# Kernel optimization log

Measured on AMD Instinct MI355X. Metric: run time of the kernel, lower is better.

## Reference

```python
import jax, jax.numpy as jnp
import numpy as np

N = 512      # num_nodes
T = 12       # seq_len
D = 1        # input_shape1
H = 64       # rnn_units
ED = 10      # units (node embedding dim)
K = 2        # cheb_k
B = 64       # batch
OUT = 1      # output_dim


def setup_inputs() -> dict:
    key = jax.random.key(0)
    ks = jax.random.split(key, 14)
    s = 0.1
    gts = jax.random.normal(ks[0], (B, N, T, D), jnp.float32)
    u = jax.random.uniform(ks[1], (N, N, 2), jnp.float32, 1e-6, 1.0 - 1e-6)
    gumbel_noise = -jnp.log(-jnp.log(u))
    node_embeddings = jax.random.normal(ks[2], (N, ED), jnp.float32)
    gate_w0 = jax.random.normal(ks[3], (ED, K, D + H, 2 * H), jnp.float32) * s
    gate_b0 = jax.random.normal(ks[4], (ED, 2 * H), jnp.float32) * s
    upd_w0 = jax.random.normal(ks[5], (ED, K, D + H, H), jnp.float32) * s
    upd_b0 = jax.random.normal(ks[6], (ED, H), jnp.float32) * s
    gate_w1 = jax.random.normal(ks[7], (ED, K, H + H, 2 * H), jnp.float32) * s
    gate_b1 = jax.random.normal(ks[8], (ED, 2 * H), jnp.float32) * s
    upd_w1 = jax.random.normal(ks[9], (ED, K, H + H, H), jnp.float32) * s
    upd_b1 = jax.random.normal(ks[10], (ED, H), jnp.float32) * s
    conv_w = jax.random.normal(ks[11], (T * OUT, H), jnp.float32) * s  # Conv2d(1, T*OUT, (1,H)) kernel flattened
    conv_b = jax.random.normal(ks[12], (T * OUT,), jnp.float32) * s
    return dict(gts=gts, gumbel_noise=gumbel_noise, node_embeddings=node_embeddings,
                gate_w0=gate_w0, gate_b0=gate_b0, upd_w0=upd_w0, upd_b0=upd_b0,
                gate_w1=gate_w1, gate_b1=gate_b1, upd_w1=upd_w1, upd_b1=upd_b1,
                conv_w=conv_w, conv_b=conv_b)


def _gconv(x, supports, E, Wp, bp):
    # x: [B,N,i], supports: [K,N,N], node-adaptive weights from pools
    xg = jnp.einsum('knm,bmi->bnki', supports, x)          # cheb graph conv
    W = jnp.einsum('nd,dkio->nkio', E, Wp)                 # per-node weights
    b = E @ bp                                             # [N,o]
    return jnp.einsum('bnki,nkio->bno', xg, W) + b


def _cell(x, h, supports, E, gw, gb, uw, ub):
    zr = jax.nn.sigmoid(_gconv(jnp.concatenate([x, h], -1), supports, E, gw, gb))
    z, r = jnp.split(zr, 2, axis=-1)
    hc = jnp.tanh(_gconv(jnp.concatenate([x, z * h], -1), supports, E, uw, ub))
    return r * h + (1.0 - r) * hc


def _scaled_laplacian(E, gumbel_noise):
    lg = E @ E.T
    nrm = jnp.linalg.norm(E, axis=1, keepdims=True)
    lg = lg / (nrm @ nrm.T)
    lg = (lg + 1.0) / 2.0
    logits = jnp.stack([lg, 1.0 - lg], axis=-1)
    y_soft = jax.nn.softmax(logits + gumbel_noise, axis=-1)  # tau=1
    y_hard = jax.nn.one_hot(jnp.argmax(y_soft, axis=-1), 2, dtype=y_soft.dtype)
    y = y_hard + y_soft - jax.lax.stop_gradient(y_soft)      # straight-through
    eye = jnp.eye(N, dtype=y.dtype)
    adj = y[..., 0] * (1.0 - eye)                            # zero diagonal
    d = adj.sum(axis=1)
    L = jnp.diag(d) - adj
    lmax = L.max() - L.min()
    tilde = 2.0 * L / lmax - eye
    return adj, tilde


def reference(gts, gumbel_noise, node_embeddings, gate_w0, gate_b0, upd_w0, upd_b0,
              gate_w1, gate_b1, upd_w1, upd_b1, conv_w, conv_b):
    E = node_embeddings
    _, tilde = _scaled_laplacian(E, gumbel_noise)
    eye = jnp.eye(N, dtype=tilde.dtype)
    supports = jnp.stack([eye, tilde])                       # cheb_k = 2
    x = jnp.transpose(gts, (0, 2, 1, 3))                     # [B,T,N,D]
    cur = jnp.moveaxis(x, 1, 0)                              # [T,B,N,D]
    b = gts.shape[0]
    for gw, gb, uw, ub in ((gate_w0, gate_b0, upd_w0, upd_b0),
                           (gate_w1, gate_b1, upd_w1, upd_b1)):
        h0 = jnp.zeros((b, N, uw.shape[-1]), dtype=gts.dtype)
        def step(h, xt, gw=gw, gb=gb, uw=uw, ub=ub):
            hn = _cell(xt, h, supports, E, gw, gb, uw, ub)
            return hn, hn
        _, cur = jax.lax.scan(step, h0, cur)                 # [T,B,N,H]
    last = cur[-1]                                           # [B,N,H] (output[:, -1])
    y = jnp.einsum('bnh,oh->bon', last, conv_w) + conv_b[None, :, None]  # end_conv
    out = y.reshape(b, T, OUT, N).transpose(0, 1, 3, 2)      # [B,T,N,OUT]
    return out
```

## Files before the change

kernel.cpp:

```cpp
#include <hip/hip_runtime.h>
#include <math.h>

#define NN 512
#define TSEQ 12
#define BB 64

typedef unsigned short u16;
typedef short s16x4 __attribute__((ext_vector_type(4)));
typedef short s16x8 __attribute__((ext_vector_type(8)));
typedef float f32x4 __attribute__((ext_vector_type(4)));

__device__ __forceinline__ float b2f(u16 h) { return __uint_as_float(((unsigned)h) << 16); }
__device__ __forceinline__ u16 f2b(float f) {
    unsigned u = __float_as_uint(f);
    return (u16)((u + 0x7FFFu + ((u >> 16) & 1u)) >> 16);
}

constexpr size_t SZP    = (size_t)512 * 4096 * 2;
constexpr size_t B_ADJ  = 0;
constexpr size_t B_DD   = B_ADJ + 524288;
constexpr size_t B_NRM  = B_DD + 2048;
constexpr size_t B_LMAX = B_NRM + 2048;
constexpr size_t B_XSH  = B_LMAX + 256;
constexpr size_t B_XSL  = B_XSH + 786432;
constexpr size_t B_TXH  = B_XSL + 786432;
constexpr size_t B_TXL  = B_TXH + 786432;
constexpr size_t B_ST   = B_TXL + 786432;
constexpr size_t B_RBUF = B_ST + 12 * SZP;
constexpr size_t B_G0TH = B_RBUF + 8388608;
constexpr size_t B_G0TL = B_G0TH + 16777216;
constexpr size_t B_U0TH = B_G0TL + 16777216;
constexpr size_t B_U0TL = B_U0TH + 8388608;
constexpr size_t B_G1TH = B_U0TL + 8388608;
constexpr size_t B_G1TL = B_G1TH + 33554432;
constexpr size_t B_U1TH = B_G1TL + 33554432;
constexpr size_t B_U1TL = B_U1TH + 16777216;
constexpr size_t B_BG0  = B_U1TL + 16777216;
constexpr size_t B_BU0  = B_BG0 + 262144;
constexpr size_t B_BG1  = B_BU0 + 131072;
constexpr size_t B_BU1  = B_BG1 + 262144;
constexpr size_t B_G0X  = B_BU1 + 131072;
constexpr size_t B_U0X  = B_G0X + 524288;
constexpr size_t WS_BYTES = B_U0X + 262144;


__global__ void k_marker(float* out, float v) { out[threadIdx.x] = v; }

__global__ void k_norm(const float* __restrict__ E, float* __restrict__ nrm) {
    int n = blockIdx.x * blockDim.x + threadIdx.x;
    if (n < NN) {
        float s = 0.f;
        #pragma unroll
        for (int q = 0; q < 10; ++q) { float e = E[n * 10 + q]; s += e * e; }
        nrm[n] = sqrtf(s);
    }
}

__global__ __launch_bounds__(256) void k_adj(const float* __restrict__ E, const float* __restrict__ gn,
                                             const float* __restrict__ nrm, u16* __restrict__ adjb,
                                             float* __restrict__ dd) {
    __shared__ float En[10];
    __shared__ float red[256];
    int n = blockIdx.x, tid = threadIdx.x;
    if (tid < 10) En[tid] = E[n * 10 + tid];
    __syncthreads();
    float nn = nrm[n];
    float cnt = 0.f;
    for (int m = tid; m < NN; m += 256) {
        float dot = 0.f;
        #pragma unroll
        for (int q = 0; q < 10; ++q) dot += En[q] * E[m * 10 + q];
        float lg = dot / (nn * nrm[m]);
        lg = (lg + 1.f) * 0.5f;
        float g0 = gn[((size_t)n * NN + m) * 2 + 0];
        float g1 = gn[((size_t)n * NN + m) * 2 + 1];
        bool a = ((lg + g0) >= (1.f - lg + g1) && (m != n));
        adjb[(size_t)n * NN + m] = a ? 0x3F80 : 0;
        cnt += a ? 1.f : 0.f;
    }
    red[tid] = cnt;
    __syncthreads();
    for (int s = 128; s > 0; s >>= 1) { if (tid < s) red[tid] += red[tid + s]; __syncthreads(); }
    if (tid == 0) dd[n] = red[0];
}

__global__ void k_dmax(const float* __restrict__ dd, float* __restrict__ lmax) {
    __shared__ float red[512];
    int t = threadIdx.x;
    red[t] = dd[t];
    __syncthreads();
    for (int s = 256; s > 0; s >>= 1) { if (t < s) red[t] = fmaxf(red[t], red[t + s]); __syncthreads(); }
    if (t == 0) lmax[0] = red[0] + (red[0] > 0.f ? 1.f : 0.f);
}

__global__ __launch_bounds__(256) void k_xs_bf(const float* __restrict__ gts, u16* __restrict__ xh,
                                               u16* __restrict__ xl) {
    int idx = blockIdx.x * 256 + threadIdx.x;
    if (idx >= NN * TSEQ * BB) return;
    int n = idx / (TSEQ * BB);
    int rem = idx - n * (TSEQ * BB);
    int t = rem >> 6, b = rem & 63;
    float v = gts[((size_t)b * NN + n) * TSEQ + t];
    u16 hb = f2b(v);
    xh[idx] = hb;
    xl[idx] = f2b(v - b2f(hb));
}

template <int K2, int O, bool SHIFT>
__global__ __launch_bounds__(256) void k_embed2(const float* __restrict__ E, const float* __restrict__ Wp,
                                                u16* __restrict__ oh, u16* __restrict__ ol) {
    constexpr int KR = SHIFT ? 130 : K2;
    constexpr int NKB = K2 / 32;
    __shared__ float WpL[10][32][33];
    __shared__ float eL[16][10];
    const int nc = blockIdx.x, kc = blockIdx.y, oc = blockIdx.z;
    const int tid = threadIdx.x;
    const int rb = kc * 32 + (SHIFT ? (kc >= 2 ? 2 : 1) : 0);
    const int ocol = oc * 32;
    const int n0 = nc * 16;

    for (int el = tid; el < 10 * 32 * 32; el += 256) {
        int d = el >> 10;
        int rem = el & 1023;
        int k = rem >> 5, o = rem & 31;
        WpL[d][k][o] = Wp[((size_t)d * KR + rb + k) * O + ocol + o];
    }
    if (tid < 160) eL[tid / 10][tid % 10] = E[(n0 + tid / 10) * 10 + tid % 10];
    __syncthreads();

    const int o2 = tid >> 3;
    const int kv = (tid & 7) * 4;
    const int o = ocol + o2;
    const int lane = ((kv >> 3) << 4) + (o & 15);
    const size_t fragbase =
        ((((size_t)0 * (O / 16) + (o >> 4)) * NKB + kc) * 64 + lane) * 8 + (kv & 7);
    const size_t nstride = (size_t)(O / 16) * NKB * 64 * 8;

    for (int ni = 0; ni < 16; ++ni) {
        float ev[10];
        #pragma unroll
        for (int d = 0; d < 10; ++d) ev[d] = eL[ni][d];
        u16 ph[4], pl[4];
        #pragma unroll
        for (int j = 0; j < 4; ++j) {
            float a = 0.f;
            #pragma unroll
            for (int d = 0; d < 10; ++d) a += ev[d] * WpL[d][kv + j][o2];
            u16 hb = f2b(a);
            ph[j] = hb;
            pl[j] = f2b(a - b2f(hb));
        }
        size_t off = fragbase + (size_t)(n0 + ni) * nstride;
        *(s16x4*)&oh[off] = *(s16x4*)ph;
        *(s16x4*)&ol[off] = *(s16x4*)pl;
    }
}

__global__ __launch_bounds__(256) void k_bias(const float* __restrict__ E, const float* __restrict__ gb0,
                                              const float* __restrict__ ub0, const float* __restrict__ gb1,
                                              const float* __restrict__ ub1, const float* __restrict__ gw0,
                                              const float* __restrict__ uw0,
                                              float* BG0, float* BU0, float* BG1, float* BU1,
                                              float* G0X, float* U0X) {
    __shared__ float e[10];
    int n = blockIdx.x, tid = threadIdx.x;
    if (tid < 10) e[tid] = E[n * 10 + tid];
    __syncthreads();
    if (tid < 128) {
        int o = tid;
        float a0 = 0, a1 = 0, a2 = 0, a3 = 0;
        #pragma unroll
        for (int d = 0; d < 10; ++d) {
            a0 += e[d] * gb0[d * 128 + o];
            a1 += e[d] * gb1[d * 128 + o];
            a2 += e[d] * gw0[((size_t)d * 130 + 0) * 128 + o];
            a3 += e[d] * gw0[((size_t)d * 130 + 65) * 128 + o];
        }
        BG0[n * 128 + o] = a0; BG1[n * 128 + o] = a1;
        G0X[n * 256 + o] = a2; G0X[n * 256 + 128 + o] = a3;
    } else if (tid < 192) {
        int o = tid - 128;
        float a0 = 0, a1 = 0, a2 = 0, a3 = 0;
        #pragma unroll
        for (int d = 0; d < 10; ++d) {
            a0 += e[d] * ub0[d * 64 + o];
            a1 += e[d] * ub1[d * 64 + o];
            a2 += e[d] * uw0[((size_t)d * 130 + 0) * 64 + o];
            a3 += e[d] * uw0[((size_t)d * 130 + 65) * 64 + o];
        }
        BU0[n * 64 + o] = a0; BU1[n * 64 + o] = a1;
        U0X[n * 128 + o] = a2; U0X[n * 128 + 64 + o] = a3;
    }
}

__global__ __launch_bounds__(256) void k_gmm(const u16* __restrict__ A, const u16* __restrict__ Bh,
                                             const u16* __restrict__ Bl, const float* __restrict__ dd,
                                             const float* __restrict__ lmax,
                                             u16* __restrict__ Ch, u16* __restrict__ Cl, int N) {
    __shared__ u16 As[2][64][72];
    __shared__ u16 Bsh[2][2][64][32];
    __shared__ u16 Bsl[2][2][64][32];
    const int tid = threadIdx.x;
    const int w = tid >> 6, l = tid & 63, lr = l & 15, lg = l >> 4;
    const int bm = blockIdx.y * 64, bn = blockIdx.x * 64;
    const int am = tid >> 2, ak = (tid & 3) * 16;
    const int bk = tid >> 3, bn8 = (tid & 7) * 8;
    const int bx = (tid & 7) & 3;
    const int col = ((bk >> 3) ^ bx) * 8 + (bk & 7);
    f32x4 acc[4];
    #pragma unroll
    for (int a = 0; a < 4; ++a) acc[a] = (f32x4){0.f, 0.f, 0.f, 0.f};

    const int nl = w * 16 + lr;
    const int cc = (lg ^ ((nl >> 3) & 3)) * 8;
    const size_t arow = (size_t)(bm + am) * 512;

    s16x8 rA0, rA1, rBh[2], rBl[2];
    rA0 = *(const s16x8*)&A[arow + 0 + ak];
    rA1 = *(const s16x8*)&A[arow + 0 + ak + 8];
    #pragma unroll
    for (int hh = 0; hh < 2; ++hh) {
        rBh[hh] = *(const s16x8*)&Bh[(size_t)(0 + hh * 32 + bk) * N + bn + bn8];
        rBl[hh] = *(const s16x8*)&Bl[(size_t)(0 + hh * 32 + bk) * N + bn + bn8];
    }
    *(s16x8*)&As[0][am][ak]     = rA0;
    *(s16x8*)&As[0][am][ak + 8] = rA1;
    #pragma unroll
    for (int hh = 0; hh < 2; ++hh) {
        #pragma unroll
        for (int q = 0; q < 8; ++q) {
            Bsh[0][hh][bn8 + q][col] = ((const u16*)&rBh[hh])[q];
            Bsl[0][hh][bn8 + q][col] = ((const u16*)&rBl[hh])[q];
        }
    }
    __syncthreads();

    for (int k0 = 0; k0 < 512; k0 += 64) {
        const int cur = (k0 >> 6) & 1;
        const bool more = (k0 + 64 < 512);
        if (more) {
            rA0 = *(const s16x8*)&A[arow + k0 + 64 + ak];
            rA1 = *(const s16x8*)&A[arow + k0 + 64 + ak + 8];
            #pragma unroll
            for (int hh = 0; hh < 2; ++hh) {
                rBh[hh] = *(const s16x8*)&Bh[(size_t)(k0 + 64 + hh * 32 + bk) * N + bn + bn8];
                rBl[hh] = *(const s16x8*)&Bl[(size_t)(k0 + 64 + hh * 32 + bk) * N + bn + bn8];
            }
        }
        #pragma unroll
        for (int hh = 0; hh < 2; ++hh) {
            s16x8 bfh = *(const s16x8*)&Bsh[cur][hh][nl][cc];
            s16x8 bfl = *(const s16x8*)&Bsl[cur][hh][nl][cc];
            #pragma unroll
            for (int mf = 0; mf < 4; ++mf) {
                s16x8 afr = *(const s16x8*)&As[cur][mf * 16 + lr][hh * 32 + lg * 8];
                acc[mf] = __builtin_amdgcn_mfma_f32_16x16x32_bf16(afr, bfh, acc[mf], 0, 0, 0);
                acc[mf] = __builtin_amdgcn_mfma_f32_16x16x32_bf16(afr, bfl, acc[mf], 0, 0, 0);
            }
        }
        if (more) {
            const int nxt = cur ^ 1;
            *(s16x8*)&As[nxt][am][ak]     = rA0;
            *(s16x8*)&As[nxt][am][ak + 8] = rA1;
            #pragma unroll
            for (int hh = 0; hh < 2; ++hh) {
                #pragma unroll
                for (int q = 0; q < 8; ++q) {
                    Bsh[nxt][hh][bn8 + q][col] = ((const u16*)&rBh[hh])[q];
                    Bsl[nxt][hh][bn8 + q][col] = ((const u16*)&rBl[hh])[q];
                }
            }
        }
        __syncthreads();
    }
    const float lm = lmax[0], alpha = -2.f / lm;
    const int colg = bn + w * 16 + lr;
    #pragma unroll
    for (int mf = 0; mf < 4; ++mf) {
        #pragma unroll
        for (int i = 0; i < 4; ++i) {
            int rowg = bm + mf * 16 + lg * 4 + i;
            size_t off = (size_t)rowg * N + colg;
            float hval = b2f(Bh[off]) + b2f(Bl[off]);
            float beta = 2.f * dd[rowg] / lm - 1.f;
            float v = alpha * acc[mf][i] + beta * hval;
            u16 hb = f2b(v);
            Ch[off] = hb;
            Cl[off] = f2b(v - b2f(hb));
        }
    }
}

struct CellP {
    const u16 *s0h, *s0l, *s1h, *s1l, *s2h, *s2l, *s3h, *s3l;
    const u16 *Wh, *Wl;
    const float *bias, *wx;
    const u16 *xsh, *xsl, *txh, *txl;
    const u16 *hph, *hpl;
    float* rbuf;
    u16 *oh, *ol;
    int xoff;
};
template <int K2, int O, bool GATE, bool RANK1>
__global__ __launch_bounds__(256) void k_cellp(CellP p) {
    constexpr int NKB = K2 / 32;
    constexpr int MFW = (O == 128) ? 4 : 2;
    const int n = blockIdx.x, tid = threadIdx.x;
    const int w = tid >> 6, l = tid & 63, lr = l & 15, lg = l >> 4;
    const int mbase = (O == 128) ? 0 : ((w >> 1) * 2);
    const int nbase = (O == 128) ? (2 * w) : ((w & 1) * 2);
    f32x4 acc[MFW][2];
    #pragma unroll
    for (int a = 0; a < MFW; ++a)
        #pragma unroll
        for (int c = 0; c < 2; ++c) acc[a][c] = (f32x4){0.f, 0.f, 0.f, 0.f};
    const size_t nb = (size_t)n * 4096;

    #pragma unroll
    for (int kb = 0; kb < NKB; ++kb) {
        const int sg = kb >> 1;
        const u16* sh = sg == 0 ? p.s0h : sg == 1 ? p.s1h : sg == 2 ? p.s2h : p.s3h;
        const u16* sl = sg == 0 ? p.s0l : sg == 1 ? p.s1l : sg == 2 ? p.s2l : p.s3l;
        const int koff = (kb & 1) * 32 + lg * 8;
        s16x8 bfh[2], bfl[2];
        #pragma unroll
        for (int nf = 0; nf < 2; ++nf) {
            size_t wof = ((((size_t)n * (O / 16) + (nbase + nf)) * NKB + kb) * 64 + l) * 8;
            bfh[nf] = *(const s16x8*)&p.Wh[wof];
            bfl[nf] = *(const s16x8*)&p.Wl[wof];
        }
        #pragma unroll
        for (int mf = 0; mf < MFW; ++mf) {
            int b = (mbase + mf) * 16 + lr;
            s16x8 ah = *(const s16x8*)&sh[nb + b * 64 + koff];
            s16x8 al = *(const s16x8*)&sl[nb + b * 64 + koff];
            #pragma unroll
            for (int nf = 0; nf < 2; ++nf) {
                acc[mf][nf] = __builtin_amdgcn_mfma_f32_16x16x32_bf16(ah, bfh[nf], acc[mf][nf], 0, 0, 0);
                acc[mf][nf] = __builtin_amdgcn_mfma_f32_16x16x32_bf16(ah, bfl[nf], acc[mf][nf], 0, 0, 0);
                acc[mf][nf] = __builtin_amdgcn_mfma_f32_16x16x32_bf16(al, bfh[nf], acc[mf][nf], 0, 0, 0);
            }
        }
    }

    const float* wxn = RANK1 ? (p.wx + (size_t)n * 2 * O) : p.wx;
    #pragma unroll
    for (int mf = 0; mf < MFW; ++mf) {
        #pragma unroll
        for (int i = 0; i < 4; ++i) {
            int b = (mbase + mf) * 16 + lg * 4 + i;
            float xf = 0.f, txf = 0.f;
            if (RANK1) {
                int idx = n * 768 + p.xoff + b;
                xf = b2f(p.xsh[idx]) + b2f(p.xsl[idx]);
                txf = b2f(p.txh[idx]) + b2f(p.txl[idx]);
            }
            #pragma unroll
            for (int nf = 0; nf < 2; ++nf) {
                int o = (nbase + nf) * 16 + lr;
                float s = acc[mf][nf][i] + p.bias[(size_t)n * O + o];
                if (RANK1) s += xf * wxn[o] + txf * wxn[O + o];
                size_t bo = nb + (size_t)b * 64;
                if (GATE) {
                    float v = 1.f / (1.f + expf(-s));
                    if (o < 64) {
                        float hp = b2f(p.hph[bo + o]) + b2f(p.hpl[bo + o]);
                        float zh = v * hp;
                        u16 hb = f2b(zh);
                        p.oh[bo + o] = hb;
                        p.ol[bo + o] = f2b(zh - b2f(hb));
                    } else {
                        p.rbuf[bo + (o - 64)] = v;
                    }
                } else {
                    float hc = tanhf(s);
                    float rv = p.rbuf[bo + o];
                    float hp = b2f(p.oh[bo + o]) + b2f(p.ol[bo + o]);
                    float hn = rv * hp + (1.f - rv) * hc;
                    u16 hb = f2b(hn);
                    p.oh[bo + o] = hb;
                    p.ol[bo + o] = f2b(hn - b2f(hb));
                }
            }
        }
    }
}

__global__ __launch_bounds__(256) void k_conv(const u16* __restrict__ hh, const u16* __restrict__ hl,
                                              const float* __restrict__ cw, const float* __restrict__ cb,
                                              float* __restrict__ out) {
    int idx = blockIdx.x * 256 + threadIdx.x;
    int n = idx >> 6, b = idx & 63;
    float hv[64];
    #pragma unroll
    for (int q = 0; q < 8; ++q) {
        s16x8 vh = *(const s16x8*)&hh[(size_t)n * 4096 + b * 64 + q * 8];
        s16x8 vl = *(const s16x8*)&hl[(size_t)n * 4096 + b * 64 + q * 8];
        #pragma unroll
        for (int j = 0; j < 8; ++j) hv[q * 8 + j] = b2f((u16)vh[j]) + b2f((u16)vl[j]);
    }
    #pragma unroll
    for (int t = 0; t < TSEQ; ++t) {
        float s = cb[t];
        #pragma unroll
        for (int j = 0; j < 64; ++j) s += hv[j] * cw[t * 64 + j];
        out[((size_t)b * TSEQ + t) * NN + n] = s;
    }
}

extern "C" void kernel_launch(void* const* d_in, const int* in_sizes, int n_in,
                              void* d_out, int out_size, void* d_ws, size_t ws_size,
                              hipStream_t stream) {
    const float* gts = (const float*)d_in[0];
    const float* gn  = (const float*)d_in[1];
    const float* E   = (const float*)d_in[2];
    const float* gw0 = (const float*)d_in[3];
    const float* gb0 = (const float*)d_in[4];
    const float* uw0 = (const float*)d_in[5];
    const float* ub0 = (const float*)d_in[6];
    const float* gw1 = (const float*)d_in[7];
    const float* gb1 = (const float*)d_in[8];
    const float* uw1 = (const float*)d_in[9];
    const float* ub1 = (const float*)d_in[10];
    const float* cw  = (const float*)d_in[11];
    const float* cb  = (const float*)d_in[12];
    float* out = (float*)d_out;
    char* ws = (char*)d_ws;

    if (ws_size < WS_BYTES) {
        k_marker<<<1, 64, 0, stream>>>(out, (float)(ws_size >> 20));
        return;
    }

    u16* adjb = (u16*)(ws + B_ADJ);
    float* dd = (float*)(ws + B_DD);
    float* nrm = (float*)(ws + B_NRM);
    float* lmax = (float*)(ws + B_LMAX);
    u16* xsh = (u16*)(ws + B_XSH);
    u16* xsl = (u16*)(ws + B_XSL);
    u16* txh = (u16*)(ws + B_TXH);
    u16* txl = (u16*)(ws + B_TXL);
    u16* h0h  = (u16*)(ws + B_ST + 0 * SZP);
    u16* h0l  = (u16*)(ws + B_ST + 1 * SZP);
    u16* h1h  = (u16*)(ws + B_ST + 2 * SZP);
    u16* h1l  = (u16*)(ws + B_ST + 3 * SZP);
    u16* th0h = (u16*)(ws + B_ST + 4 * SZP);
    u16* th0l = (u16*)(ws + B_ST + 5 * SZP);
    u16* th1h = (u16*)(ws + B_ST + 6 * SZP);
    u16* th1l = (u16*)(ws + B_ST + 7 * SZP);
    u16* zhh  = (u16*)(ws + B_ST + 8 * SZP);
    u16* zhl  = (u16*)(ws + B_ST + 9 * SZP);
    u16* tzh  = (u16*)(ws + B_ST + 10 * SZP);
    u16* tzl  = (u16*)(ws + B_ST + 11 * SZP);
    float* rbuf = (float*)(ws + B_RBUF);
    u16* G0TH = (u16*)(ws + B_G0TH);
    u16* G0TL = (u16*)(ws + B_G0TL);
    u16* U0TH = (u16*)(ws + B_U0TH);
    u16* U0TL = (u16*)(ws + B_U0TL);
    u16* G1TH = (u16*)(ws + B_G1TH);
    u16* G1TL = (u16*)(ws + B_G1TL);
    u16* U1TH = (u16*)(ws + B_U1TH);
    u16* U1TL = (u16*)(ws + B_U1TL);
    float* BG0 = (float*)(ws + B_BG0);
    float* BU0 = (float*)(ws + B_BU0);
    float* BG1 = (float*)(ws + B_BG1);
    float* BU1 = (float*)(ws + B_BU1);
    float* G0X = (float*)(ws + B_G0X);
    float* U0X = (float*)(ws + B_U0X);

    hipMemsetAsync(ws, 0, WS_BYTES, stream);

    k_norm<<<2, 256, 0, stream>>>(E, nrm);
    k_adj<<<NN, 256, 0, stream>>>(E, gn, nrm, adjb, dd);
    k_dmax<<<1, 512, 0, stream>>>(dd, lmax);

    k_xs_bf<<<(NN * TSEQ * BB + 255) / 256, 256, 0, stream>>>(gts, xsh, xsl);
    k_gmm<<<dim3(TSEQ * BB / 64, 8), 256, 0, stream>>>(adjb, xsh, xsl, dd, lmax, txh, txl, TSEQ * BB);

    k_embed2<128, 128, true><<<dim3(32, 4, 4), 256, 0, stream>>>(E, gw0, G0TH, G0TL);
    k_embed2<128, 64, true><<<dim3(32, 4, 2), 256, 0, stream>>>(E, uw0, U0TH, U0TL);
    k_embed2<256, 128, false><<<dim3(32, 8, 4), 256, 0, stream>>>(E, gw1, G1TH, G1TL);
    k_embed2<256, 64, false><<<dim3(32, 8, 2), 256, 0, stream>>>(E, uw1, U1TH, U1TL);
    k_bias<<<512, 256, 0, stream>>>(E, gb0, ub0, gb1, ub1, gw0, uw0,
                                    BG0, BU0, BG1, BU1, G0X, U0X);

    const dim3 gmm_grid(BB * 64 / 64, 8);
    for (int t = 0; t < TSEQ; ++t) {
        int xoff = t * BB;
        CellP g0{h0h, h0l, th0h, th0l, nullptr, nullptr, nullptr, nullptr,
                 G0TH, G0TL, BG0, G0X, xsh, xsl, txh, txl, h0h, h0l, rbuf, zhh, zhl, xoff};
        k_cellp<128, 128, true, true><<<NN, 256, 0, stream>>>(g0);
        k_gmm<<<gmm_grid, 256, 0, stream>>>(adjb, zhh, zhl, dd, lmax, tzh, tzl, 4096);
        CellP u0{zhh, zhl, tzh, tzl, nullptr, nullptr, nullptr, nullptr,
                 U0TH, U0TL, BU0, U0X, xsh, xsl, txh, txl, nullptr, nullptr, rbuf, h0h, h0l, xoff};
        k_cellp<128, 64, false, true><<<NN, 256, 0, stream>>>(u0);
        k_gmm<<<gmm_grid, 256, 0, stream>>>(adjb, h0h, h0l, dd, lmax, th0h, th0l, 4096);
        CellP g1{h0h, h0l, h1h, h1l, th0h, th0l, th1h, th1l,
                 G1TH, G1TL, BG1, nullptr, nullptr, nullptr, nullptr, nullptr, h1h, h1l, rbuf, zhh, zhl, 0};
        k_cellp<256, 128, true, false><<<NN, 256, 0, stream>>>(g1);
        k_gmm<<<gmm_grid, 256, 0, stream>>>(adjb, zhh, zhl, dd, lmax, tzh, tzl, 4096);
        CellP u1{h0h, h0l, zhh, zhl, th0h, th0l, tzh, tzl,
                 U1TH, U1TL, BU1, nullptr, nullptr, nullptr, nullptr, nullptr, nullptr, nullptr, rbuf, h1h, h1l, 0};
        k_cellp<256, 64, false, false><<<NN, 256, 0, stream>>>(u1);
        if (t + 1 < TSEQ)
            k_gmm<<<gmm_grid, 256, 0, stream>>>(adjb, h1h, h1l, dd, lmax, th1h, th1l, 4096);
    }

    k_conv<<<NN * BB / 256, 256, 0, stream>>>(h1h, h1l, cw, cb, out);
}
```

Measured before the change: 1.942 ms.

## Fuse layer-1 hidden graph conv with next step's layer-0 gate cell

Wraps the GEMM and cell kernels as device functions and adds a combined kernel. Its first 512 blocks compute the support product of the layer-1 hidden state, and the remaining 512 blocks compute the next timestep's layer-0 gate cell. The two are independent, so this removes one launch per step and lets them overlap on the GPU. The cell blocks now reserve the GEMM's shared memory even though they don't use it, which may reduce occupancy.

```diff
diff --git a/kernel.cpp b/kernel.cpp
--- a/kernel.cpp
+++ b/kernel.cpp
@@ -193,16 +193,19 @@
     }
 }
 
-__global__ __launch_bounds__(256) void k_gmm(const u16* __restrict__ A, const u16* __restrict__ Bh,
-                                             const u16* __restrict__ Bl, const float* __restrict__ dd,
-                                             const float* __restrict__ lmax,
-                                             u16* __restrict__ Ch, u16* __restrict__ Cl, int N) {
-    __shared__ u16 As[2][64][72];
-    __shared__ u16 Bsh[2][2][64][32];
-    __shared__ u16 Bsl[2][2][64][32];
-    const int tid = threadIdx.x;
+struct GmmS {
+    u16 As[2][64][72];
+    u16 Bsh[2][2][64][32];
+    u16 Bsl[2][2][64][32];
+};
+
+__device__ __forceinline__ void d_gmm(int by, int bx_, int tid,
+                                      const u16* __restrict__ A, const u16* __restrict__ Bh,
+                                      const u16* __restrict__ Bl, const float* __restrict__ dd,
+                                      const float* __restrict__ lmax,
+                                      u16* __restrict__ Ch, u16* __restrict__ Cl, int N, GmmS& S) {
     const int w = tid >> 6, l = tid & 63, lr = l & 15, lg = l >> 4;
-    const int bm = blockIdx.y * 64, bn = blockIdx.x * 64;
+    const int bm = by * 64, bn = bx_ * 64;
     const int am = tid >> 2, ak = (tid & 3) * 16;
     const int bk = tid >> 3, bn8 = (tid & 7) * 8;
     const int bx = (tid & 7) & 3;
@@ -223,14 +226,14 @@
         rBh[hh] = *(const s16x8*)&Bh[(size_t)(0 + hh * 32 + bk) * N + bn + bn8];
         rBl[hh] = *(const s16x8*)&Bl[(size_t)(0 + hh * 32 + bk) * N + bn + bn8];
     }
-    *(s16x8*)&As[0][am][ak]     = rA0;
-    *(s16x8*)&As[0][am][ak + 8] = rA1;
+    *(s16x8*)&S.As[0][am][ak]     = rA0;
+    *(s16x8*)&S.As[0][am][ak + 8] = rA1;
     #pragma unroll
     for (int hh = 0; hh < 2; ++hh) {
         #pragma unroll
         for (int q = 0; q < 8; ++q) {
-            Bsh[0][hh][bn8 + q][col] = ((const u16*)&rBh[hh])[q];
-            Bsl[0][hh][bn8 + q][col] = ((const u16*)&rBl[hh])[q];
+            S.Bsh[0][hh][bn8 + q][col] = ((const u16*)&rBh[hh])[q];
+            S.Bsl[0][hh][bn8 + q][col] = ((const u16*)&rBl[hh])[q];
         }
     }
     __syncthreads();
@@ -249,25 +252,25 @@
         }
         #pragma unroll
         for (int hh = 0; hh < 2; ++hh) {
-            s16x8 bfh = *(const s16x8*)&Bsh[cur][hh][nl][cc];
-            s16x8 bfl = *(const s16x8*)&Bsl[cur][hh][nl][cc];
+            s16x8 bfh = *(const s16x8*)&S.Bsh[cur][hh][nl][cc];
+            s16x8 bfl = *(const s16x8*)&S.Bsl[cur][hh][nl][cc];
             #pragma unroll
             for (int mf = 0; mf < 4; ++mf) {
-                s16x8 afr = *(const s16x8*)&As[cur][mf * 16 + lr][hh * 32 + lg * 8];
+                s16x8 afr = *(const s16x8*)&S.As[cur][mf * 16 + lr][hh * 32 + lg * 8];
                 acc[mf] = __builtin_amdgcn_mfma_f32_16x16x32_bf16(afr, bfh, acc[mf], 0, 0, 0);
                 acc[mf] = __builtin_amdgcn_mfma_f32_16x16x32_bf16(afr, bfl, acc[mf], 0, 0, 0);
             }
         }
         if (more) {
             const int nxt = cur ^ 1;
-            *(s16x8*)&As[nxt][am][ak]     = rA0;
-            *(s16x8*)&As[nxt][am][ak + 8] = rA1;
+            *(s16x8*)&S.As[nxt][am][ak]     = rA0;
+            *(s16x8*)&S.As[nxt][am][ak + 8] = rA1;
             #pragma unroll
             for (int hh = 0; hh < 2; ++hh) {
                 #pragma unroll
                 for (int q = 0; q < 8; ++q) {
-                    Bsh[nxt][hh][bn8 + q][col] = ((const u16*)&rBh[hh])[q];
-                    Bsl[nxt][hh][bn8 + q][col] = ((const u16*)&rBl[hh])[q];
+                    S.Bsh[nxt][hh][bn8 + q][col] = ((const u16*)&rBh[hh])[q];
+                    S.Bsl[nxt][hh][bn8 + q][col] = ((const u16*)&rBl[hh])[q];
                 }
             }
         }
@@ -289,6 +292,14 @@
             Cl[off] = f2b(v - b2f(hb));
         }
     }
+}
+
+__global__ __launch_bounds__(256) void k_gmm(const u16* __restrict__ A, const u16* __restrict__ Bh,
+                                             const u16* __restrict__ Bl, const float* __restrict__ dd,
+                                             const float* __restrict__ lmax,
+                                             u16* __restrict__ Ch, u16* __restrict__ Cl, int N) {
+    __shared__ GmmS S;
+    d_gmm(blockIdx.y, blockIdx.x, threadIdx.x, A, Bh, Bl, dd, lmax, Ch, Cl, N, S);
 }
 
 struct CellP {
@@ -302,10 +313,9 @@
     int xoff;
 };
 template <int K2, int O, bool GATE, bool RANK1>
-__global__ __launch_bounds__(256) void k_cellp(CellP p) {
+__device__ __forceinline__ void d_cellp(int n, int tid, const CellP& p) {
     constexpr int NKB = K2 / 32;
     constexpr int MFW = (O == 128) ? 4 : 2;
-    const int n = blockIdx.x, tid = threadIdx.x;
     const int w = tid >> 6, l = tid & 63, lr = l & 15, lg = l >> 4;
     const int mbase = (O == 128) ? 0 : ((w >> 1) * 2);
     const int nbase = (O == 128) ? (2 * w) : ((w & 1) * 2);
@@ -386,6 +396,27 @@
     }
 }
 
+template <int K2, int O, bool GATE, bool RANK1>
+__global__ __launch_bounds__(256) void k_cellp(CellP p) {
+    d_cellp<K2, O, GATE, RANK1>(blockIdx.x, threadIdx.x, p);
+}
+
+struct FuseArgs {
+    const u16* adjb; const u16 *h1h, *h1l; const float *dd, *lmax;
+    u16 *th1h, *th1l;
+    CellP cell;
+};
+__global__ __launch_bounds__(256) void k_fuse(FuseArgs a) {
+    __shared__ GmmS S;
+    const int bid = blockIdx.x;
+    if (bid < 512) {
+        d_gmm(bid >> 6, bid & 63, threadIdx.x, a.adjb, a.h1h, a.h1l, a.dd, a.lmax,
+              a.th1h, a.th1l, 4096, S);
+    } else {
+        d_cellp<128, 128, true, true>(bid - 512, threadIdx.x, a.cell);
+    }
+}
+
 __global__ __launch_bounds__(256) void k_conv(const u16* __restrict__ hh, const u16* __restrict__ hl,
                                               const float* __restrict__ cw, const float* __restrict__ cb,
                                               float* __restrict__ out) {
@@ -487,9 +518,11 @@
     const dim3 gmm_grid(BB * 64 / 64, 8);
     for (int t = 0; t < TSEQ; ++t) {
         int xoff = t * BB;
-        CellP g0{h0h, h0l, th0h, th0l, nullptr, nullptr, nullptr, nullptr,
-                 G0TH, G0TL, BG0, G0X, xsh, xsl, txh, txl, h0h, h0l, rbuf, zhh, zhl, xoff};
-        k_cellp<128, 128, true, true><<<NN, 256, 0, stream>>>(g0);
+        if (t == 0) {
+            CellP g0{h0h, h0l, th0h, th0l, nullptr, nullptr, nullptr, nullptr,
+                     G0TH, G0TL, BG0, G0X, xsh, xsl, txh, txl, h0h, h0l, rbuf, zhh, zhl, xoff};
+            k_cellp<128, 128, true, true><<<NN, 256, 0, stream>>>(g0);
+        }
         k_gmm<<<gmm_grid, 256, 0, stream>>>(adjb, zhh, zhl, dd, lmax, tzh, tzl, 4096);
         CellP u0{zhh, zhl, tzh, tzl, nullptr, nullptr, nullptr, nullptr,
                  U0TH, U0TL, BU0, U0X, xsh, xsl, txh, txl, nullptr, nullptr, rbuf, h0h, h0l, xoff};
@@ -502,8 +535,12 @@
         CellP u1{h0h, h0l, zhh, zhl, th0h, th0l, tzh, tzl,
                  U1TH, U1TL, BU1, nullptr, nullptr, nullptr, nullptr, nullptr, nullptr, nullptr, rbuf, h1h, h1l, 0};
         k_cellp<256, 64, false, false><<<NN, 256, 0, stream>>>(u1);
-        if (t + 1 < TSEQ)
-            k_gmm<<<gmm_grid, 256, 0, stream>>>(adjb, h1h, h1l, dd, lmax, th1h, th1l, 4096);
+        if (t + 1 < TSEQ) {
+            CellP g0n{h0h, h0l, th0h, th0l, nullptr, nullptr, nullptr, nullptr,
+                      G0TH, G0TL, BG0, G0X, xsh, xsl, txh, txl, h0h, h0l, rbuf, zhh, zhl, (t + 1) * BB};
+            FuseArgs fa{adjb, h1h, h1l, dd, lmax, th1h, th1l, g0n};
+            k_fuse<<<1024, 256, 0, stream>>>(fa);
+        }
     }
 
     k_conv<<<NN * BB / 256, 256, 0, stream>>>(h1h, h1l, cw, cb, out);
```

Measured after the change: 1.864 ms. 4.0% less time.
